# Performance work log

Measured on AMD Instinct MI355X. Metric: run time of the kernel, lower is better.

The kernel has to match this reference:

```python
import jax, jax.numpy as jnp
import numpy as np

DIM = 2048
H = 16
KV_RANK = 512
NOPE = 128
ROPE_D = 64
VD = 128
QK = NOPE + ROPE_D  # 192
SCALE = QK ** -0.5
B, S = 2, 2048
EPS = 1e-5


def _rope(x, start_pos):
    # x: (b, s, h, d) or (b, s, d); rotate along last dim, positions along axis 1
    s = x.shape[1]
    d = x.shape[-1]
    half = d // 2
    inv_freq = 1.0 / (10000.0 ** (jnp.arange(half, dtype=jnp.float32) * (2.0 / d)))
    pos = jnp.arange(start_pos, start_pos + s, dtype=jnp.float32)
    ang = pos[:, None] * inv_freq[None, :]  # (s, half)
    cos, sin = jnp.cos(ang), jnp.sin(ang)
    if x.ndim == 4:
        cos, sin = cos[None, :, None, :], sin[None, :, None, :]
    else:
        cos, sin = cos[None, :, :], sin[None, :, :]
    x1, x2 = x[..., :half], x[..., half:]
    return jnp.concatenate([x1 * cos - x2 * sin, x2 * cos + x1 * sin], axis=-1).astype(x.dtype)


def _layernorm(x, w, b):
    mu = jnp.mean(x, axis=-1, keepdims=True)
    var = jnp.mean(jnp.square(x - mu), axis=-1, keepdims=True)
    return (x - mu) * jax.lax.rsqrt(var + EPS) * w + b


def setup_inputs() -> dict:
    key = jax.random.key(0)
    ks = jax.random.split(key, 6)
    std = 0.02
    x = jax.random.normal(ks[0], (B, S, DIM), dtype=jnp.float32)
    wq = jax.random.normal(ks[1], (H * QK, DIM), dtype=jnp.float32) * std
    wkv_a = jax.random.normal(ks[2], (KV_RANK + ROPE_D, DIM), dtype=jnp.float32) * std
    wkv_b = jax.random.normal(ks[3], (H * (NOPE + VD), KV_RANK), dtype=jnp.float32) * std
    wo = jax.random.normal(ks[4], (DIM, H * VD), dtype=jnp.float32) * std
    kv_norm_w = jnp.ones((KV_RANK,), dtype=jnp.float32)
    kv_norm_b = jnp.zeros((KV_RANK,), dtype=jnp.float32)
    return {"x": x, "wq": wq, "wkv_a": wkv_a, "kv_norm_w": kv_norm_w,
            "kv_norm_b": kv_norm_b, "wkv_b": wkv_b, "wo": wo, "start_pos": 0}


def reference(x, wq, wkv_a, kv_norm_w, kv_norm_b, wkv_b, wo, start_pos):
    b, s, _ = x.shape
    # query projection: (b,s,H,QK)
    q = (x @ wq.T).reshape(b, s, H, QK)
    q_nope, q_pe = q[..., :NOPE], q[..., NOPE:]
    q_pe = _rope(q_pe, start_pos)
    # compressed kv + rope key
    kv_all = x @ wkv_a.T                      # (b,s,KV_RANK+ROPE_D)
    kv, k_pe = kv_all[..., :KV_RANK], kv_all[..., KV_RANK:]
    k_pe = _rope(k_pe, start_pos)             # (b,s,ROPE_D)
    kvn = _layernorm(kv, kv_norm_w, kv_norm_b)  # (b,s,KV_RANK)
    # absorb path: expand compressed kv through per-head wkv_b blocks
    w = wkv_b.reshape(H, NOPE + VD, KV_RANK)
    k_nope = jnp.einsum('btc,hdc->bthd', kvn, w[:, :NOPE])   # (b,t,H,NOPE)
    v = jnp.einsum('btc,hdc->bthd', kvn, w[:, NOPE:])        # (b,t,H,VD)
    q_full = jnp.concatenate([q_nope, q_pe], axis=-1)        # (b,s,H,QK)
    k_full = jnp.concatenate(
        [k_nope, jnp.broadcast_to(k_pe[:, :, None, :], (b, s, H, ROPE_D))], axis=-1)
    scores = jnp.einsum('bshd,bthd->bhst', q_full, k_full) * SCALE
    causal = jnp.tril(jnp.ones((s, s), dtype=bool))
    scores = jnp.where(causal[None, None], scores, jnp.float32(-1e30))
    attn = jax.nn.softmax(scores, axis=-1)
    out = jnp.einsum('bhst,bthd->bshd', attn, v).reshape(b, s, H * VD)
    return out @ wo.T
```

## Files before the change

### kernel.cpp

```cpp
#include <hip/hip_runtime.h>
#include <hip/hip_bf16.h>
#include <math.h>

typedef __bf16 bf16_t;
typedef __bf16 bf16x2 __attribute__((ext_vector_type(2)));
typedef __bf16 bf16x4 __attribute__((ext_vector_type(4)));
typedef __bf16 bf16x8 __attribute__((ext_vector_type(8)));
typedef float f32x4 __attribute__((ext_vector_type(4)));

#define SEQ 2048
#define MLA_SCALE 0.07216878364870322f
#define LN_EPS 1e-5f

__device__ __forceinline__ void gload_lds16(const bf16_t* g, bf16_t* l) {
    __builtin_amdgcn_global_load_lds(
        (const __attribute__((address_space(1))) uint32_t*)(const void*)g,
        (__attribute__((address_space(3))) uint32_t*)(void*)l, 16, 0, 0);
}

__device__ __forceinline__ void xcd_map(int bid, int total, int nbn,
                                        int& bm, int& bn) {
    int per = total >> 3;
    int cbm = per / nbn;
    int xcd = bid & 7, s = bid >> 3;
    int q = s / nbn;
    bm = xcd * cbm + q;
    bn = s - q * nbn;
}

#define CVT_N0 2097152
#define CVT_N1 1572864
#define CVT_N2 294912
#define CVT_N3 524288
#define CVT_N4 1048576
#define CVT_TOT (CVT_N0 + CVT_N1 + CVT_N2 + CVT_N3 + CVT_N4)

__global__ __launch_bounds__(256)
void cvt_all(const float* __restrict__ x, const float* __restrict__ wq,
             const float* __restrict__ wa, const float* __restrict__ wb,
             const float* __restrict__ wo, bf16_t* __restrict__ xb,
             bf16_t* __restrict__ wqb, bf16_t* __restrict__ wab,
             bf16_t* __restrict__ wbb, bf16_t* __restrict__ wob) {
    for (int i = blockIdx.x * 256 + threadIdx.x; i < CVT_TOT; i += gridDim.x * 256) {
        const float* src; bf16_t* dst; int off = i;
        if (i < CVT_N0) { src = x; dst = xb; }
        else if (i < CVT_N0 + CVT_N1) { src = wq; dst = wqb; off = i - CVT_N0; }
        else if (i < CVT_N0 + CVT_N1 + CVT_N2) { src = wa; dst = wab; off = i - CVT_N0 - CVT_N1; }
        else if (i < CVT_N0 + CVT_N1 + CVT_N2 + CVT_N3) { src = wb; dst = wbb; off = i - CVT_N0 - CVT_N1 - CVT_N2; }
        else { src = wo; dst = wob; off = i - CVT_N0 - CVT_N1 - CVT_N2 - CVT_N3; }
        float4 v = ((const float4*)src)[off];
        bf16x4 p = { (bf16_t)v.x, (bf16_t)v.y, (bf16_t)v.z, (bf16_t)v.w };
        ((bf16x4*)dst)[off] = p;
    }
}

#define G256_PHASE(TAU, KS, MH, HTO, MAT, WAITV)                               \
{                                                                              \
    const int slot_ = (2 * (TAU) + (KS)) & 3;                                  \
    bf16x8 af_[4];                                                             \
    {                                                                          \
        const bf16_t* ab_ = As + slot_ * 8192 +                                \
                            (wm2 * 128 + (MH) * 64 + lr) * 32 + rdcol;         \
        _Pragma("unroll")                                                      \
        for (int f = 0; f < 4; ++f) af_[f] = *(const bf16x8*)(ab_ + f * 512);  \
    }                                                                          \
    if ((MH) == 0) {                                                           \
        const bf16_t* bb_ = Bs + slot_ * 8192 + (wn2 * 64 + lr) * 32 + rdcol;  \
        _Pragma("unroll")                                                      \
        for (int f = 0; f < 4; ++f) bq[f] = *(const bf16x8*)(bb_ + f * 512);   \
    }                                                                          \
    if ((MAT) == 0) stageA(2 * T + 3 + (HTO)); else stageB(2 * T + 3 + (HTO)); \
    __builtin_amdgcn_s_barrier();                                              \
    asm volatile("" ::: "memory");                                             \
    __builtin_amdgcn_s_setprio(1);                                             \
    _Pragma("unroll")                                                          \
    for (int f = 0; f < 4; ++f)                                                \
        _Pragma("unroll")                                                      \
        for (int n = 0; n < 4; ++n)                                            \
            acc[(MH) * 4 + f][n] = __builtin_amdgcn_mfma_f32_16x16x32_bf16(    \
                af_[f], bq[n], acc[(MH) * 4 + f][n], 0, 0, 0);                 \
    __builtin_amdgcn_s_setprio(0);                                             \
    asm volatile("" ::: "memory");                                             \
    if (WAITV) asm volatile("s_waitcnt vmcnt(8)" ::: "memory");                \
    __builtin_amdgcn_s_barrier();                                              \
}

template<int MODE>
__global__ __launch_bounds__(512, 2)
void gemm256(const bf16_t* __restrict__ A, const bf16_t* __restrict__ B,
             float* __restrict__ C, bf16_t* __restrict__ out0,
             bf16_t* __restrict__ out1, int N, int K, int total, int nbn) {
    __shared__ __attribute__((aligned(16))) bf16_t As[32768];
    __shared__ __attribute__((aligned(16))) bf16_t Bs[32768];
    __shared__ __attribute__((aligned(16))) bf16_t Ds[8192];

    const int tid = threadIdx.x;
    const int lane = tid & 63, w = tid >> 6;
    const int lr = lane & 15, kh = lane >> 4;
    const int wm2 = w >> 2, wn2 = w & 3;
    int bm, bn;
    xcd_map(blockIdx.x, total, nbn, bm, bn);
    const int NT = K >> 6;

    const int rdcol = 8 * (kh ^ ((lr >> 1) & 3));
    const int strow = (w << 5) + (lane >> 2);
    const int scol = 8 * ((lane & 3) ^ ((lane >> 3) & 3));

    f32x4 acc[8][4];
    #pragma unroll
    for (int i = 0; i < 8; ++i)
        #pragma unroll
        for (int j = 0; j < 4; ++j) acc[i][j] = 0.0f;

    auto stageA = [&](int ht) {
        int hs = (ht < 2 * NT) ? ht : (2 * NT - 1);
        int tau = hs >> 1, kap = hs & 1;
        const bf16_t* g = A + (size_t)(bm * 256 + strow) * K + tau * 64 + kap * 32 + scol;
        bf16_t* l = (ht < 2 * NT) ? (As + (ht & 3) * 8192 + w * 1024) : (Ds + w * 1024);
        gload_lds16(g, l);
        gload_lds16(g + (size_t)16 * K, l + 512);
    };
    auto stageB = [&](int ht) {
        int hs = (ht < 2 * NT) ? ht : (2 * NT - 1);
        int tau = hs >> 1, kap = hs & 1;
        const bf16_t* g = B + (size_t)(bn * 256 + strow) * K + tau * 64 + kap * 32 + scol;
        bf16_t* l = (ht < 2 * NT) ? (Bs + (ht & 3) * 8192 + w * 1024) : (Ds + w * 1024);
        gload_lds16(g, l);
        gload_lds16(g + (size_t)16 * K, l + 512);
    };

    stageA(0); stageB(0); stageA(1); stageB(1); stageA(2); stageB(2);
    asm volatile("s_waitcnt vmcnt(8)" ::: "memory");
    __builtin_amdgcn_s_barrier();

    for (int it = 0; it < (NT >> 1); ++it) {
        const int T = 2 * it;
        bf16x8 bq[4];
        G256_PHASE(T,     0, 0, 0, 0, 0)
        G256_PHASE(T,     0, 1, 0, 1, 1)
        G256_PHASE(T,     1, 0, 1, 0, 0)
        G256_PHASE(T,     1, 1, 1, 1, 1)
        G256_PHASE(T + 1, 0, 0, 2, 0, 0)
        G256_PHASE(T + 1, 0, 1, 2, 1, 1)
        G256_PHASE(T + 1, 1, 0, 3, 0, 0)
        G256_PHASE(T + 1, 1, 1, 3, 1, 1)
    }

    const int rg = kh * 4;
    if (MODE == 0) {
        #pragma unroll
        for (int mf = 0; mf < 8; ++mf)
            #pragma unroll
            for (int nf = 0; nf < 4; ++nf) {
                size_t row0 = (size_t)(bm * 256 + wm2 * 128 + mf * 16 + rg);
                int col = bn * 256 + wn2 * 64 + nf * 16 + lr;
                #pragma unroll
                for (int rr = 0; rr < 4; ++rr)
                    C[(row0 + rr) * N + col] = acc[mf][nf][rr];
            }
    } else if (MODE == 1) {
        const int h = bn;
        #pragma unroll
        for (int mf = 0; mf < 8; ++mf)
            #pragma unroll
            for (int nf = 0; nf < 4; ++nf) {
                int d = wn2 * 64 + nf * 16 + lr;
                int trow = bm * 256 + wm2 * 128 + mf * 16 + rg;
                int b = trow >> 11, t = trow & 2047;
                if (d < 128) {
                    bf16_t* p = out0 + ((size_t)(b * 16 + h) * SEQ + t) * 192 + d;
                    #pragma unroll
                    for (int rr = 0; rr < 4; ++rr)
                        p[rr * 192] = (bf16_t)acc[mf][nf][rr];
                } else {
                    bf16x4 pv = { (bf16_t)acc[mf][nf][0], (bf16_t)acc[mf][nf][1],
                                  (bf16_t)acc[mf][nf][2], (bf16_t)acc[mf][nf][3] };
                    *(bf16x4*)(out1 + ((size_t)(b * 16 + h) * 128 + (d - 128)) * SEQ + t) = pv;
                }
            }
    } else {
        #pragma unroll
        for (int mf = 0; mf < 8; ++mf)
            #pragma unroll
            for (int nf = 0; nf < 4; ++nf) {
                int n = bn * 256 + wn2 * 64 + nf * 16 + lr;
                int h = n / 192, d = n - h * 192;
                int trow = bm * 256 + wm2 * 128 + mf * 16 + rg;
                int b = trow >> 11, t = trow & 2047;
                bf16_t* p = out0 + ((size_t)(b * 16 + h) * SEQ + t) * 192 + d;
                #pragma unroll
                for (int rr = 0; rr < 4; ++rr)
                    p[rr * 192] = (bf16_t)acc[mf][nf][rr];
            }
    }
}

__global__ __launch_bounds__(256)
void gemm_nt(const bf16_t* __restrict__ A, const bf16_t* __restrict__ B,
             float* __restrict__ C, int M, int N, int K, int total, int nbn) {
    __shared__ bf16_t As[4096], Bs[4096];
    int bm, bn;
    xcd_map(blockIdx.x, total, nbn, bm, bn);

    const int tid = threadIdx.x;
    const int lane = tid & 63, w = tid >> 6;
    const int lr = lane & 15, kh = lane >> 4;
    const int wm = (w >> 1) * 64, wn = (w & 1) * 64;
    const int subrow = lane >> 2;
    const int colel = (lane & 3) * 8;

    f32x4 acc[4][4];
    #pragma unroll
    for (int i = 0; i < 4; ++i)
        #pragma unroll
        for (int j = 0; j < 4; ++j) acc[i][j] = 0.0f;

    const int rA = bm * 128 + 32 * w + subrow;
    const int rB = bn * 128 + 32 * w + subrow;
    const int rb1 = (rB < N) ? rB : (N - 1);
    const int rb2 = (rB + 16 < N) ? (rB + 16) : (N - 1);

    for (int kt = 0; kt < K; kt += 32) {
        __syncthreads();
        gload_lds16(A + (size_t)rA * K + kt + colel,        As + (2 * w) * 512);
        gload_lds16(A + (size_t)(rA + 16) * K + kt + colel, As + (2 * w + 1) * 512);
        gload_lds16(B + (size_t)rb1 * K + kt + colel,       Bs + (2 * w) * 512);
        gload_lds16(B + (size_t)rb2 * K + kt + colel,       Bs + (2 * w + 1) * 512);
        __syncthreads();
        bf16x8 af[4], bfr[4];
        #pragma unroll
        for (int im = 0; im < 4; ++im)
            af[im] = *(const bf16x8*)(As + (wm + im * 16 + lr) * 32 + kh * 8);
        #pragma unroll
        for (int jn = 0; jn < 4; ++jn)
            bfr[jn] = *(const bf16x8*)(Bs + (wn + jn * 16 + lr) * 32 + kh * 8);
        #pragma unroll
        for (int im = 0; im < 4; ++im)
            #pragma unroll
            for (int jn = 0; jn < 4; ++jn)
                acc[im][jn] = __builtin_amdgcn_mfma_f32_16x16x32_bf16(
                    af[im], bfr[jn], acc[im][jn], 0, 0, 0);
    }

    const int rg = kh * 4;
    #pragma unroll
    for (int im = 0; im < 4; ++im)
        #pragma unroll
        for (int jn = 0; jn < 4; ++jn) {
            int col = bn * 128 + wn + jn * 16 + lr;
            if (col >= N) continue;
            size_t rowb = (size_t)(bm * 128 + wm + im * 16 + rg);
            #pragma unroll
            for (int rr = 0; rr < 4; ++rr)
                C[(rowb + rr) * N + col] = acc[im][jn][rr];
        }
}

__global__ __launch_bounds__(256)
void rope_ln(const float* __restrict__ kv_all,
             const float* __restrict__ lnw, const float* __restrict__ lnb,
             bf16_t* __restrict__ kvnb, bf16_t* __restrict__ kpack,
             float2* __restrict__ rope_cs, const int* __restrict__ start_pos) {
    const int m = blockIdx.x;
    const int tid = threadIdx.x;
    const int b = m >> 11, t = m & 2047;
    const float pos = (float)(start_pos[0] + t);
    __shared__ float red[8];
    __shared__ float stats[2];
    __shared__ float kbuf[64];

    const float* kvrow = kv_all + (size_t)m * 576;
    float v0 = kvrow[tid], v1 = kvrow[tid + 256];
    float ssum = v0 + v1, ssq = v0 * v0 + v1 * v1;
    for (int off = 32; off > 0; off >>= 1) {
        ssum += __shfl_down(ssum, off);
        ssq  += __shfl_down(ssq, off);
    }
    const int lane = tid & 63, wid = tid >> 6;
    if (lane == 0) { red[wid] = ssum; red[4 + wid] = ssq; }
    __syncthreads();
    if (tid == 0) {
        float ts = red[0] + red[1] + red[2] + red[3];
        float tq = red[4] + red[5] + red[6] + red[7];
        float mu = ts * (1.0f / 512.0f);
        float var = tq * (1.0f / 512.0f) - mu * mu;
        stats[0] = mu;
        stats[1] = rsqrtf(var + LN_EPS);
    }
    if (tid < 32) {
        int j = tid;
        float inv = expf(-(float)j * 0.2878231366242554f);
        float ang = pos * inv;
        float c = cosf(ang), sn = sinf(ang);
        float x1 = kvrow[512 + j], x2 = kvrow[544 + j];
        kbuf[j]      = x1 * c - x2 * sn;
        kbuf[32 + j] = x2 * c + x1 * sn;
        if (b == 0) rope_cs[t * 32 + j] = make_float2(c, sn);
    }
    __syncthreads();
    float mu = stats[0], rstd = stats[1];
    kvnb[(size_t)m * 512 + tid]       = (bf16_t)((v0 - mu) * rstd * lnw[tid] + lnb[tid]);
    kvnb[(size_t)m * 512 + tid + 256] = (bf16_t)((v1 - mu) * rstd * lnw[tid + 256] + lnb[tid + 256]);

    {
        int hh = tid >> 4, j4 = (tid & 15) * 4;
        bf16x4 pk = { (bf16_t)kbuf[j4], (bf16_t)kbuf[j4 + 1],
                      (bf16_t)kbuf[j4 + 2], (bf16_t)kbuf[j4 + 3] };
        *(bf16x4*)(kpack + ((size_t)(b * 16 + hh) * SEQ + t) * 192 + 128 + j4) = pk;
    }
}

__global__ __launch_bounds__(128)
void attn_mfma(const bf16_t* __restrict__ qb, const bf16_t* __restrict__ kpack,
               const bf16_t* __restrict__ vt, const float2* __restrict__ rope_cs,
               bf16_t* __restrict__ ao) {
    __shared__ __attribute__((aligned(16))) bf16_t Ks[2][64 * 192];
    __shared__ __attribute__((aligned(16))) bf16_t Vts[128 * 64];
    __shared__ __attribute__((aligned(16))) bf16_t Pls[2 * 32 * 64];

    const int bid = blockIdx.x;
    const int xcd = bid & 7, s = bid >> 3;
    const int grp = xcd * 4 + (s >> 4);
    const int bx = s & 15;
    const int h = grp & 15, b = grp >> 4;

    const int tid = threadIdx.x;
    const int lane = tid & 63, w = tid >> 6;
    const int lr = lane & 15, kh = lane >> 4;
    const int lr7 = lr & 7;
    const int e0 = kh ^ lr7;
    const int e1 = (4 + kh) ^ lr7;
    const size_t bS = (size_t)b * SEQ;
    const bf16_t* kbase = kpack + (size_t)(b * 16 + h) * SEQ * 192;
    const bf16_t* vbase = vt + (size_t)(b * 16 + h) * 128 * SEQ;

    int kgo_[12];
    #pragma unroll
    for (int i = 0; i < 12; ++i) {
        int c = tid + 128 * i;
        int row = c / 24, sl = c % 24;
        kgo_[i] = row * 192 + ((sl & 24) | ((sl ^ row) & 7)) * 8;
    }
    int vgo_[8];
    #pragma unroll
    for (int i = 0; i < 8; ++i) {
        int c = tid + 128 * i;
        int d = c >> 3, sl = c & 7;
        vgo_[i] = d * SEQ + ((sl ^ (d & 7)) * 8);
    }

    for (int half = 0; half < 2; ++half) {
        const int qt = half ? bx : (31 - bx);
        const int q0 = qt * 64;
        int qabs[2];
        qabs[0] = q0 + w * 32 + lr;
        qabs[1] = q0 + w * 32 + 16 + lr;

        bf16x8 qf[2][6];
        #pragma unroll
        for (int g = 0; g < 2; ++g) {
            const bf16_t* qrow = qb + ((size_t)(b * 16 + h) * SEQ + qabs[g]) * 192;
            #pragma unroll
            for (int ks = 0; ks < 6; ++ks)
                qf[g][ks] = *(const bf16x8*)(qrow + ks * 32 + kh * 8);
            const float2* csp = rope_cs + (size_t)qabs[g] * 32 + kh * 8;
            #pragma unroll
            for (int i = 0; i < 8; ++i) {
                float2 cs = csp[i];
                float x1 = (float)qf[g][4][i], x2 = (float)qf[g][5][i];
                qf[g][4][i] = (bf16_t)(x1 * cs.x - x2 * cs.y);
                qf[g][5][i] = (bf16_t)(x2 * cs.x + x1 * cs.y);
            }
        }

        f32x4 O[2][8];
        #pragma unroll
        for (int g = 0; g < 2; ++g)
            #pragma unroll
            for (int i = 0; i < 8; ++i) O[g][i] = 0.0f;
        float m_r[2] = { -1e30f, -1e30f }, l_r[2] = { 0.0f, 0.0f };

        int cur = 0;
        #pragma unroll
        for (int i = 0; i < 12; ++i)
            gload_lds16(kbase + kgo_[i], Ks[0] + (128 * i + 64 * w) * 8);
        asm volatile("s_waitcnt vmcnt(0)" ::: "memory");
        __syncthreads();

        for (int kt = 0; kt <= qt; ++kt) {
            bf16_t* kcur = Ks[cur];
            bf16_t* knxt = Ks[cur ^ 1];
            #pragma unroll
            for (int i = 0; i < 8; ++i)
                gload_lds16(vbase + vgo_[i] + kt * 64, Vts + (128 * i + 64 * w) * 8);
            const int tn = (kt + 1 <= qt) ? (kt + 1) : qt;
            #pragma unroll
            for (int i = 0; i < 12; ++i)
                gload_lds16(kbase + (size_t)tn * 12288 + kgo_[i],
                            knxt + (128 * i + 64 * w) * 8);

            f32x4 sacc[2][4];
            #pragma unroll
            for (int g = 0; g < 2; ++g)
                #pragma unroll
                for (int j = 0; j < 4; ++j) sacc[g][j] = 0.0f;
            __builtin_amdgcn_s_setprio(1);
            #pragma unroll
            for (int ks = 0; ks < 6; ++ks) {
                const int sw = (ks >> 1) * 64 + ((ks & 1) ? e1 : e0) * 8;
                #pragma unroll
                for (int j = 0; j < 4; ++j) {
                    bf16x8 kf = *(const bf16x8*)(kcur + (j * 16 + lr) * 192 + sw);
                    sacc[0][j] = __builtin_amdgcn_mfma_f32_16x16x32_bf16(kf, qf[0][ks], sacc[0][j], 0, 0, 0);
                    sacc[1][j] = __builtin_amdgcn_mfma_f32_16x16x32_bf16(kf, qf[1][ks], sacc[1][j], 0, 0, 0);
                }
            }
            __builtin_amdgcn_s_setprio(0);

            const int t0 = kt * 64;
            const int f2 = kh >> 1, h4 = (kh & 1) * 4;
            #pragma unroll
            for (int g = 0; g < 2; ++g) {
                float p[16];
                if (kt == qt) {
                    #pragma unroll
                    for (int j = 0; j < 4; ++j)
                        #pragma unroll
                        for (int rr = 0; rr < 4; ++rr) {
                            int tabs = t0 + j * 16 + kh * 4 + rr;
                            p[j * 4 + rr] = (tabs > qabs[g]) ? -1e30f
                                           : sacc[g][j][rr] * MLA_SCALE;
                        }
                } else {
                    #pragma unroll
                    for (int j = 0; j < 4; ++j)
                        #pragma unroll
                        for (int rr = 0; rr < 4; ++rr)
                            p[j * 4 + rr] = sacc[g][j][rr] * MLA_SCALE;
                }

                float mx = p[0];
                #pragma unroll
                for (int e = 1; e < 16; ++e) mx = fmaxf(mx, p[e]);
                mx = fmaxf(mx, __shfl_xor(mx, 16));
                mx = fmaxf(mx, __shfl_xor(mx, 32));

                if (!__all(mx <= m_r[g] + 8.0f)) {
                    float mnew = fmaxf(m_r[g], mx);
                    float cr = __expf(m_r[g] - mnew);
                    l_r[g] *= cr;
                    m_r[g] = mnew;
                    float corr[4];
                    #pragma unroll
                    for (int rr = 0; rr < 4; ++rr)
                        corr[rr] = __shfl(cr, kh * 4 + rr);
                    #pragma unroll
                    for (int dt = 0; dt < 8; ++dt)
                        #pragma unroll
                        for (int rr = 0; rr < 4; ++rr)
                            O[g][dt][rr] *= corr[rr];
                }

                float ps = 0.0f;
                #pragma unroll
                for (int e = 0; e < 16; ++e) {
                    p[e] = __expf(p[e] - m_r[g]);
                    ps += p[e];
                }
                ps += __shfl_xor(ps, 16);
                ps += __shfl_xor(ps, 32);
                l_r[g] += ps;

                bf16_t* pw = Pls + (w * 32 + g * 16 + lr) * 64;
                #pragma unroll
                for (int j = 0; j < 4; ++j) {
                    bf16x4 pp = { (bf16_t)p[j * 4], (bf16_t)p[j * 4 + 1],
                                  (bf16_t)p[j * 4 + 2], (bf16_t)p[j * 4 + 3] };
                    *(bf16x4*)(pw + ((2 * j + f2) ^ lr7) * 8 + h4) = pp;
                }
            }

            asm volatile("s_waitcnt vmcnt(12)" ::: "memory");
            __syncthreads();

            bf16x8 pa[2][2];
            #pragma unroll
            for (int g = 0; g < 2; ++g) {
                const bf16_t* pw = Pls + (w * 32 + g * 16 + lr) * 64;
                pa[g][0] = *(const bf16x8*)(pw + e0 * 8);
                pa[g][1] = *(const bf16x8*)(pw + e1 * 8);
            }
            __builtin_amdgcn_s_setprio(1);
            #pragma unroll
            for (int dt = 0; dt < 8; ++dt) {
                bf16x8 b0 = *(const bf16x8*)(Vts + (dt * 16 + lr) * 64 + e0 * 8);
                bf16x8 b1 = *(const bf16x8*)(Vts + (dt * 16 + lr) * 64 + e1 * 8);
                O[0][dt] = __builtin_amdgcn_mfma_f32_16x16x32_bf16(pa[0][0], b0, O[0][dt], 0, 0, 0);
                O[0][dt] = __builtin_amdgcn_mfma_f32_16x16x32_bf16(pa[0][1], b1, O[0][dt], 0, 0, 0);
                O[1][dt] = __builtin_amdgcn_mfma_f32_16x16x32_bf16(pa[1][0], b0, O[1][dt], 0, 0, 0);
                O[1][dt] = __builtin_amdgcn_mfma_f32_16x16x32_bf16(pa[1][1], b1, O[1][dt], 0, 0, 0);
            }
            __builtin_amdgcn_s_setprio(0);

            asm volatile("s_waitcnt vmcnt(0)" ::: "memory");
            __syncthreads();
            cur ^= 1;
        }

        #pragma unroll
        for (int g = 0; g < 2; ++g) {
            float linv[4];
            #pragma unroll
            for (int rr = 0; rr < 4; ++rr)
                linv[rr] = 1.0f / __shfl(l_r[g], kh * 4 + rr);
            #pragma unroll
            for (int rr = 0; rr < 4; ++rr) {
                size_t rowb = (bS + q0 + w * 32 + g * 16 + kh * 4 + rr) * 2048 + h * 128;
                #pragma unroll
                for (int dt = 0; dt < 8; ++dt)
                    ao[rowb + dt * 16 + lr] = (bf16_t)(O[g][dt][rr] * linv[rr]);
            }
        }
        __syncthreads();
    }
}

extern "C" void kernel_launch(void* const* d_in, const int* in_sizes, int n_in,
                              void* d_out, int out_size, void* d_ws, size_t ws_size,
                              hipStream_t stream) {
    const float* x     = (const float*)d_in[0];
    const float* wq    = (const float*)d_in[1];
    const float* wkv_a = (const float*)d_in[2];
    const float* lnw   = (const float*)d_in[3];
    const float* lnb   = (const float*)d_in[4];
    const float* wkv_b = (const float*)d_in[5];
    const float* wo    = (const float*)d_in[6];
    const int* start_pos = (const int*)d_in[7];
    float* out = (float*)d_out;

    char* w8 = (char*)d_ws;
    bf16_t* xb   = (bf16_t*)(w8);
    bf16_t* wqb  = (bf16_t*)(w8 + 16777216);
    bf16_t* wab  = (bf16_t*)(w8 + 29360128);
    bf16_t* wbb  = (bf16_t*)(w8 + 31719424);
    bf16_t* wob  = (bf16_t*)(w8 + 35913728);
    bf16_t* kvnb = (bf16_t*)(w8 + 44302336);
    bf16_t* kpk  = (bf16_t*)(w8 + 48496640);
    bf16_t* vtb  = (bf16_t*)(w8 + 73662464);
    bf16_t* aob  = (bf16_t*)(w8 + 90439680);
    bf16_t* qbh  = (bf16_t*)(w8 + 107216896);
    float*  kva  = (float*)(w8 + 132382720);
    float2* rcs  = (float2*)(w8 + 141819904);

    cvt_all<<<2048, 256, 0, stream>>>(x, wq, wkv_a, wkv_b, wo, xb, wqb, wab, wbb, wob);

    gemm256<2><<<192, 512, 0, stream>>>(xb, wqb, nullptr, qbh, nullptr, 3072, 2048, 192, 12);
    gemm_nt<<<160, 256, 0, stream>>>(xb, wab, kva, 4096, 576, 2048, 160, 5);
    rope_ln<<<4096, 256, 0, stream>>>(kva, lnw, lnb, kvnb, kpk, rcs, start_pos);
    gemm256<1><<<256, 512, 0, stream>>>(kvnb, wbb, nullptr, kpk, vtb, 4096, 512, 256, 16);
    attn_mfma<<<512, 128, 0, stream>>>(qbh, kpk, vtb, rcs, aob);
    gemm_nt<<<512, 256, 0, stream>>>(aob, wob, out, 4096, 2048, 2048, 512, 16);
}
```

Measured before the change: 305.4 us.

## Split attention KV tile across four waves with LDS-shared softmax stats

The attention kernel goes from 128 to 256 threads. For QK, each pair of waves handles half of the 64-key tile for 32 query rows. Row max and row sum are combined across wave pairs through small shared-memory arrays, adding one extra barrier per tile. For PV, each wave owns 16 query rows. V tiles are now prefetched into registers and written to LDS manually instead of using direct global-to-LDS loads, and the output rescale now runs on every tile rather than being skipped conditionally. The aim is more waves per CU and fewer registers per wave, at the cost of extra synchronisation.

```diff
diff --git a/kernel.cpp b/kernel.cpp
--- a/kernel.cpp
+++ b/kernel.cpp
@@ -310,13 +310,15 @@
     }
 }
 
-__global__ __launch_bounds__(128)
+__global__ __launch_bounds__(256, 2)
 void attn_mfma(const bf16_t* __restrict__ qb, const bf16_t* __restrict__ kpack,
                const bf16_t* __restrict__ vt, const float2* __restrict__ rope_cs,
                bf16_t* __restrict__ ao) {
     __shared__ __attribute__((aligned(16))) bf16_t Ks[2][64 * 192];
     __shared__ __attribute__((aligned(16))) bf16_t Vts[128 * 64];
-    __shared__ __attribute__((aligned(16))) bf16_t Pls[2 * 32 * 64];
+    __shared__ __attribute__((aligned(16))) bf16_t Pls[64 * 64];
+    __shared__ float pmls[2][64];
+    __shared__ float psls[2][64];
 
     const int bid = blockIdx.x;
     const int xcd = bid & 7, s = bid >> 3;
@@ -328,42 +330,42 @@
     const int lane = tid & 63, w = tid >> 6;
     const int lr = lane & 15, kh = lane >> 4;
     const int lr7 = lr & 7;
+    const int tq = w & 1, qh = w >> 1;
     const int e0 = kh ^ lr7;
     const int e1 = (4 + kh) ^ lr7;
     const size_t bS = (size_t)b * SEQ;
     const bf16_t* kbase = kpack + (size_t)(b * 16 + h) * SEQ * 192;
     const bf16_t* vbase = vt + (size_t)(b * 16 + h) * 128 * SEQ;
 
-    int kgo_[12];
+    int kgo_[6];
     #pragma unroll
-    for (int i = 0; i < 12; ++i) {
-        int c = tid + 128 * i;
+    for (int i = 0; i < 6; ++i) {
+        int c = (i * 4 + w) * 64 + lane;
         int row = c / 24, sl = c % 24;
         kgo_[i] = row * 192 + ((sl & 24) | ((sl ^ row) & 7)) * 8;
     }
-    int vgo_[8];
+    int vgo_[4], vlo_[4];
     #pragma unroll
-    for (int i = 0; i < 8; ++i) {
-        int c = tid + 128 * i;
+    for (int i = 0; i < 4; ++i) {
+        int c = tid + 256 * i;
         int d = c >> 3, sl = c & 7;
-        vgo_[i] = d * SEQ + ((sl ^ (d & 7)) * 8);
+        vgo_[i] = d * SEQ + sl * 8;
+        vlo_[i] = d * 64 + ((sl ^ (d & 7)) * 8);
     }
 
     for (int half = 0; half < 2; ++half) {
         const int qt = half ? bx : (31 - bx);
         const int q0 = qt * 64;
-        int qabs[2];
-        qabs[0] = q0 + w * 32 + lr;
-        qabs[1] = q0 + w * 32 + 16 + lr;
 
         bf16x8 qf[2][6];
         #pragma unroll
         for (int g = 0; g < 2; ++g) {
-            const bf16_t* qrow = qb + ((size_t)(b * 16 + h) * SEQ + qabs[g]) * 192;
+            const int qa = q0 + qh * 32 + g * 16 + lr;
+            const bf16_t* qrow = qb + ((size_t)(b * 16 + h) * SEQ + qa) * 192;
             #pragma unroll
             for (int ks = 0; ks < 6; ++ks)
                 qf[g][ks] = *(const bf16x8*)(qrow + ks * 32 + kh * 8);
-            const float2* csp = rope_cs + (size_t)qabs[g] * 32 + kh * 8;
+            const float2* csp = rope_cs + (size_t)qa * 32 + kh * 8;
             #pragma unroll
             for (int i = 0; i < 8; ++i) {
                 float2 cs = csp[i];
@@ -373,153 +375,178 @@
             }
         }
 
-        f32x4 O[2][8];
-        #pragma unroll
-        for (int g = 0; g < 2; ++g)
-            #pragma unroll
-            for (int i = 0; i < 8; ++i) O[g][i] = 0.0f;
-        float m_r[2] = { -1e30f, -1e30f }, l_r[2] = { 0.0f, 0.0f };
+        f32x4 O[8];
+        #pragma unroll
+        for (int i = 0; i < 8; ++i) O[i] = 0.0f;
+        float m_qk[2] = { -1e30f, -1e30f };
+        float l_r = 0.0f;
 
         int cur = 0;
         #pragma unroll
-        for (int i = 0; i < 12; ++i)
-            gload_lds16(kbase + kgo_[i], Ks[0] + (128 * i + 64 * w) * 8);
-        asm volatile("s_waitcnt vmcnt(0)" ::: "memory");
+        for (int i = 0; i < 6; ++i)
+            gload_lds16(kbase + kgo_[i], Ks[0] + (i * 4 + w) * 512);
+        bf16x8 rv[4];
+        #pragma unroll
+        for (int i = 0; i < 4; ++i)
+            rv[i] = *(const bf16x8*)(vbase + vgo_[i]);
         __syncthreads();
 
         for (int kt = 0; kt <= qt; ++kt) {
-            bf16_t* kcur = Ks[cur];
-            bf16_t* knxt = Ks[cur ^ 1];
-            #pragma unroll
-            for (int i = 0; i < 8; ++i)
-                gload_lds16(vbase + vgo_[i] + kt * 64, Vts + (128 * i + 64 * w) * 8);
-            const int tn = (kt + 1 <= qt) ? (kt + 1) : qt;
-            #pragma unroll
-            for (int i = 0; i < 12; ++i)
-                gload_lds16(kbase + (size_t)tn * 12288 + kgo_[i],
-                            knxt + (128 * i + 64 * w) * 8);
-
-            f32x4 sacc[2][4];
-            #pragma unroll
-            for (int g = 0; g < 2; ++g)
-                #pragma unroll
-                for (int j = 0; j < 4; ++j) sacc[g][j] = 0.0f;
+            const bf16_t* kcur = Ks[cur];
+            if (kt < qt) {
+                #pragma unroll
+                for (int i = 0; i < 6; ++i)
+                    gload_lds16(kbase + (size_t)(kt + 1) * 12288 + kgo_[i],
+                                Ks[cur ^ 1] + (i * 4 + w) * 512);
+            }
+
+            f32x4 sacc[2][2];
+            #pragma unroll
+            for (int tj = 0; tj < 2; ++tj)
+                #pragma unroll
+                for (int g = 0; g < 2; ++g) sacc[tj][g] = 0.0f;
             __builtin_amdgcn_s_setprio(1);
             #pragma unroll
             for (int ks = 0; ks < 6; ++ks) {
                 const int sw = (ks >> 1) * 64 + ((ks & 1) ? e1 : e0) * 8;
                 #pragma unroll
-                for (int j = 0; j < 4; ++j) {
-                    bf16x8 kf = *(const bf16x8*)(kcur + (j * 16 + lr) * 192 + sw);
-                    sacc[0][j] = __builtin_amdgcn_mfma_f32_16x16x32_bf16(kf, qf[0][ks], sacc[0][j], 0, 0, 0);
-                    sacc[1][j] = __builtin_amdgcn_mfma_f32_16x16x32_bf16(kf, qf[1][ks], sacc[1][j], 0, 0, 0);
+                for (int tj = 0; tj < 2; ++tj) {
+                    bf16x8 kf = *(const bf16x8*)(kcur + (tq * 32 + tj * 16 + lr) * 192 + sw);
+                    sacc[tj][0] = __builtin_amdgcn_mfma_f32_16x16x32_bf16(kf, qf[0][ks], sacc[tj][0], 0, 0, 0);
+                    sacc[tj][1] = __builtin_amdgcn_mfma_f32_16x16x32_bf16(kf, qf[1][ks], sacc[tj][1], 0, 0, 0);
                 }
             }
             __builtin_amdgcn_s_setprio(0);
 
             const int t0 = kt * 64;
-            const int f2 = kh >> 1, h4 = (kh & 1) * 4;
-            #pragma unroll
-            for (int g = 0; g < 2; ++g) {
-                float p[16];
-                if (kt == qt) {
+            float p[2][2][4];
+            if (kt == qt) {
+                #pragma unroll
+                for (int tj = 0; tj < 2; ++tj)
                     #pragma unroll
-                    for (int j = 0; j < 4; ++j)
+                    for (int g = 0; g < 2; ++g)
                         #pragma unroll
                         for (int rr = 0; rr < 4; ++rr) {
-                            int tabs = t0 + j * 16 + kh * 4 + rr;
-                            p[j * 4 + rr] = (tabs > qabs[g]) ? -1e30f
-                                           : sacc[g][j][rr] * MLA_SCALE;
+                            int tabs = t0 + tq * 32 + tj * 16 + kh * 4 + rr;
+                            int qa = q0 + qh * 32 + g * 16 + lr;
+                            p[tj][g][rr] = (tabs > qa) ? -1e30f : sacc[tj][g][rr] * MLA_SCALE;
                         }
-                } else {
+            } else {
+                #pragma unroll
+                for (int tj = 0; tj < 2; ++tj)
                     #pragma unroll
-                    for (int j = 0; j < 4; ++j)
+                    for (int g = 0; g < 2; ++g)
                         #pragma unroll
                         for (int rr = 0; rr < 4; ++rr)
-                            p[j * 4 + rr] = sacc[g][j][rr] * MLA_SCALE;
-                }
-
-                float mx = p[0];
-                #pragma unroll
-                for (int e = 1; e < 16; ++e) mx = fmaxf(mx, p[e]);
+                            p[tj][g][rr] = sacc[tj][g][rr] * MLA_SCALE;
+            }
+
+            float pmax[2];
+            #pragma unroll
+            for (int g = 0; g < 2; ++g) {
+                float mx = p[0][g][0];
+                #pragma unroll
+                for (int e = 1; e < 4; ++e) mx = fmaxf(mx, p[0][g][e]);
+                #pragma unroll
+                for (int e = 0; e < 4; ++e) mx = fmaxf(mx, p[1][g][e]);
                 mx = fmaxf(mx, __shfl_xor(mx, 16));
                 mx = fmaxf(mx, __shfl_xor(mx, 32));
-
-                if (!__all(mx <= m_r[g] + 8.0f)) {
-                    float mnew = fmaxf(m_r[g], mx);
-                    float cr = __expf(m_r[g] - mnew);
-                    l_r[g] *= cr;
-                    m_r[g] = mnew;
-                    float corr[4];
+                pmax[g] = mx;
+            }
+            if (kh == 0) {
+                pmls[tq][qh * 32 + lr] = pmax[0];
+                pmls[tq][qh * 32 + 16 + lr] = pmax[1];
+            }
+            __syncthreads();
+
+            float cr[2];
+            #pragma unroll
+            for (int g = 0; g < 2; ++g) {
+                int q2 = qh * 32 + g * 16 + lr;
+                float mx2 = fmaxf(pmls[0][q2], pmls[1][q2]);
+                float mn = (mx2 > m_qk[g] + 8.0f) ? mx2 : m_qk[g];
+                cr[g] = __expf(m_qk[g] - mn);
+                m_qk[g] = mn;
+            }
+            float crp = cr[w & 1];
+            l_r *= crp;
+            float corr[4];
+            #pragma unroll
+            for (int rr = 0; rr < 4; ++rr)
+                corr[rr] = __shfl(crp, kh * 4 + rr);
+            #pragma unroll
+            for (int dt = 0; dt < 8; ++dt)
+                #pragma unroll
+                for (int rr = 0; rr < 4; ++rr)
+                    O[dt][rr] *= corr[rr];
+
+            float ps2[2] = { 0.0f, 0.0f };
+            #pragma unroll
+            for (int tj = 0; tj < 2; ++tj)
+                #pragma unroll
+                for (int g = 0; g < 2; ++g)
                     #pragma unroll
-                    for (int rr = 0; rr < 4; ++rr)
-                        corr[rr] = __shfl(cr, kh * 4 + rr);
-                    #pragma unroll
-                    for (int dt = 0; dt < 8; ++dt)
-                        #pragma unroll
-                        for (int rr = 0; rr < 4; ++rr)
-                            O[g][dt][rr] *= corr[rr];
+                    for (int rr = 0; rr < 4; ++rr) {
+                        float e = __expf(p[tj][g][rr] - m_qk[g]);
+                        p[tj][g][rr] = e;
+                        ps2[g] += e;
+                    }
+            #pragma unroll
+            for (int g = 0; g < 2; ++g) {
+                ps2[g] += __shfl_xor(ps2[g], 16);
+                ps2[g] += __shfl_xor(ps2[g], 32);
+            }
+            if (kh == 0) {
+                psls[tq][qh * 32 + lr] = ps2[0];
+                psls[tq][qh * 32 + 16 + lr] = ps2[1];
+            }
+            #pragma unroll
+            for (int tj = 0; tj < 2; ++tj)
+                #pragma unroll
+                for (int g = 0; g < 2; ++g) {
+                    int q2 = qh * 32 + g * 16 + lr;
+                    int slot = tq * 4 + tj * 2 + (kh >> 1);
+                    bf16x4 pp = { (bf16_t)p[tj][g][0], (bf16_t)p[tj][g][1],
+                                  (bf16_t)p[tj][g][2], (bf16_t)p[tj][g][3] };
+                    *(bf16x4*)(Pls + q2 * 64 + ((slot ^ lr7) * 8) + (kh & 1) * 4) = pp;
                 }
-
-                float ps = 0.0f;
-                #pragma unroll
-                for (int e = 0; e < 16; ++e) {
-                    p[e] = __expf(p[e] - m_r[g]);
-                    ps += p[e];
-                }
-                ps += __shfl_xor(ps, 16);
-                ps += __shfl_xor(ps, 32);
-                l_r[g] += ps;
-
-                bf16_t* pw = Pls + (w * 32 + g * 16 + lr) * 64;
-                #pragma unroll
-                for (int j = 0; j < 4; ++j) {
-                    bf16x4 pp = { (bf16_t)p[j * 4], (bf16_t)p[j * 4 + 1],
-                                  (bf16_t)p[j * 4 + 2], (bf16_t)p[j * 4 + 3] };
-                    *(bf16x4*)(pw + ((2 * j + f2) ^ lr7) * 8 + h4) = pp;
-                }
-            }
-
-            asm volatile("s_waitcnt vmcnt(12)" ::: "memory");
+            #pragma unroll
+            for (int i = 0; i < 4; ++i) *(bf16x8*)(Vts + vlo_[i]) = rv[i];
             __syncthreads();
 
-            bf16x8 pa[2][2];
-            #pragma unroll
-            for (int g = 0; g < 2; ++g) {
-                const bf16_t* pw = Pls + (w * 32 + g * 16 + lr) * 64;
-                pa[g][0] = *(const bf16x8*)(pw + e0 * 8);
-                pa[g][1] = *(const bf16x8*)(pw + e1 * 8);
-            }
+            if (kt < qt) {
+                #pragma unroll
+                for (int i = 0; i < 4; ++i)
+                    rv[i] = *(const bf16x8*)(vbase + vgo_[i] + (kt + 1) * 64);
+            }
+
+            const bf16_t* pw = Pls + (w * 16 + lr) * 64;
+            bf16x8 pa0 = *(const bf16x8*)(pw + e0 * 8);
+            bf16x8 pa1 = *(const bf16x8*)(pw + e1 * 8);
             __builtin_amdgcn_s_setprio(1);
             #pragma unroll
             for (int dt = 0; dt < 8; ++dt) {
                 bf16x8 b0 = *(const bf16x8*)(Vts + (dt * 16 + lr) * 64 + e0 * 8);
+                O[dt] = __builtin_amdgcn_mfma_f32_16x16x32_bf16(pa0, b0, O[dt], 0, 0, 0);
                 bf16x8 b1 = *(const bf16x8*)(Vts + (dt * 16 + lr) * 64 + e1 * 8);
-                O[0][dt] = __builtin_amdgcn_mfma_f32_16x16x32_bf16(pa[0][0], b0, O[0][dt], 0, 0, 0);
-                O[0][dt] = __builtin_amdgcn_mfma_f32_16x16x32_bf16(pa[0][1], b1, O[0][dt], 0, 0, 0);
-                O[1][dt] = __builtin_amdgcn_mfma_f32_16x16x32_bf16(pa[1][0], b0, O[1][dt], 0, 0, 0);
-                O[1][dt] = __builtin_amdgcn_mfma_f32_16x16x32_bf16(pa[1][1], b1, O[1][dt], 0, 0, 0);
+                O[dt] = __builtin_amdgcn_mfma_f32_16x16x32_bf16(pa1, b1, O[dt], 0, 0, 0);
             }
             __builtin_amdgcn_s_setprio(0);
 
-            asm volatile("s_waitcnt vmcnt(0)" ::: "memory");
-            __syncthreads();
+            l_r += psls[0][w * 16 + lr] + psls[1][w * 16 + lr];
             cur ^= 1;
         }
 
-        #pragma unroll
-        for (int g = 0; g < 2; ++g) {
-            float linv[4];
-            #pragma unroll
-            for (int rr = 0; rr < 4; ++rr)
-                linv[rr] = 1.0f / __shfl(l_r[g], kh * 4 + rr);
-            #pragma unroll
-            for (int rr = 0; rr < 4; ++rr) {
-                size_t rowb = (bS + q0 + w * 32 + g * 16 + kh * 4 + rr) * 2048 + h * 128;
-                #pragma unroll
-                for (int dt = 0; dt < 8; ++dt)
-                    ao[rowb + dt * 16 + lr] = (bf16_t)(O[g][dt][rr] * linv[rr]);
-            }
+        float linv[4];
+        #pragma unroll
+        for (int rr = 0; rr < 4; ++rr)
+            linv[rr] = 1.0f / __shfl(l_r, kh * 4 + rr);
+        #pragma unroll
+        for (int rr = 0; rr < 4; ++rr) {
+            size_t rowb = (bS + q0 + w * 16 + kh * 4 + rr) * 2048 + h * 128;
+            #pragma unroll
+            for (int dt = 0; dt < 8; ++dt)
+                ao[rowb + dt * 16 + lr] = (bf16_t)(O[dt][rr] * linv[rr]);
         }
         __syncthreads();
     }
@@ -558,6 +585,6 @@
     gemm_nt<<<160, 256, 0, stream>>>(xb, wab, kva, 4096, 576, 2048, 160, 5);
     rope_ln<<<4096, 256, 0, stream>>>(kva, lnw, lnb, kvnb, kpk, rcs, start_pos);
     gemm256<1><<<256, 512, 0, stream>>>(kvnb, wbb, nullptr, kpk, vtb, 4096, 512, 256, 16);
-    attn_mfma<<<512, 128, 0, stream>>>(qbh, kpk, vtb, rcs, aob);
+    attn_mfma<<<512, 256, 0, stream>>>(qbh, kpk, vtb, rcs, aob);
     gemm_nt<<<512, 256, 0, stream>>>(aob, wob, out, 4096, 2048, 2048, 512, 16);
 }
```

New measurement: 285.2 us. -6.6%, faster.
